# Performance work log

Hardware: AMD Instinct MI355X
Metric: run time of the kernel (lower is better)

The kernel has to match this reference:

```python
import jax, jax.numpy as jnp
import numpy as np

N, F, E, D, H, G = 65536, 256, 16, 256, 512, 256  # nodes, feat, experts(node_num), emb_dim, hidden_dim, graphs


def setup_inputs() -> dict:
    key = jax.random.key(0)
    ks = jax.random.split(key, 11)
    scale = 0.02
    return {
        "node_fea": jax.random.normal(ks[0], (N, F), jnp.float32),
        "masks": jax.random.uniform(ks[1], (N, F), jnp.float32),
        "node_type": jax.random.randint(ks[2], (N,), 0, E),
        "g_node_id": jnp.sort(jax.random.randint(ks[3], (G,), 0, N)),
        "label": jax.random.randint(ks[4], (G,), 0, 2),
        "W_emb": jax.random.normal(ks[5], (E, F, D), jnp.float32) * scale,
        "b_emb": jax.random.normal(ks[6], (E, D), jnp.float32) * scale,
        "W_hid": jax.random.normal(ks[7], (D, H), jnp.float32) * scale,
        "b_hid": jax.random.normal(ks[8], (H,), jnp.float32) * scale,
        "W_out": jax.random.normal(ks[9], (H, 2), jnp.float32) * scale,
        "b_out": jax.random.normal(ks[10], (2,), jnp.float32) * scale,
    }


def reference(node_fea, masks, node_type, g_node_id, label,
              W_emb, b_emb, W_hid, b_hid, W_out, b_out):
    # --- node_embedding: per-node type-routed linear (grouped GEMM form) ---
    xm = node_fea * masks                                   # [N, F]
    # run every expert densely, then select each node's expert output
    all_emb = jnp.einsum('nf,efd->ned', xm, W_emb) + b_emb[None]   # [N, E, D]
    emb = jnp.take_along_axis(all_emb, node_type[:, None, None], axis=1)[:, 0, :]  # [N, D]
    # --- hidden_fc (dropout in eval mode = identity) ---
    h = emb @ W_hid + b_hid                                 # [N, H]
    # --- pick first node of each batched graph ---
    g_emb = h[g_node_id]                                    # [G, H]
    # --- output layer: Linear + Softmax ---
    probs = jax.nn.softmax(g_emb @ W_out + b_out, axis=-1)  # [G, 2]
    # --- CrossEntropyLoss(reduction='sum') applied to probs (as in source) ---
    logp = jax.nn.log_softmax(probs, axis=-1)
    loss = -jnp.sum(jnp.take_along_axis(logp, label[:, None], axis=1))
    return probs, loss
```

## Files before the change

### kernel.cpp

```cpp
#include <hip/hip_runtime.h>
#include <math.h>

#define FF 256
#define EE 16
#define DD 256
#define HH 512
#define GG 256

__global__ __launch_bounds__(256) void fused_graph_kernel(
    const float* __restrict__ node_fea,
    const float* __restrict__ masks,
    const int*   __restrict__ node_type,
    const int*   __restrict__ g_node_id,
    const int*   __restrict__ label,
    const float* __restrict__ W_emb,
    const float* __restrict__ b_emb,
    const float* __restrict__ W_hid,
    const float* __restrict__ b_hid,
    const float* __restrict__ W_out,
    const float* __restrict__ b_out,
    float* __restrict__ probs_out,
    float* __restrict__ loss_ws)
{
    __shared__ float xm[FF];
    __shared__ float emb[DD];
    __shared__ float red0[4];
    __shared__ float red1[4];

    const int g = blockIdx.x;
    const int t = threadIdx.x;
    const int n = g_node_id[g];
    const int e = node_type[n];

    {
        size_t base = (size_t)n * FF + t;
        xm[t] = node_fea[base] * masks[base];
    }
    __syncthreads();

    {
        const float* __restrict__ W = W_emb + (size_t)e * FF * DD + t;
        float acc = b_emb[e * DD + t];
        #pragma unroll 8
        for (int f = 0; f < FF; ++f) {
            acc = fmaf(xm[f], W[(size_t)f * DD], acc);
        }
        emb[t] = acc;
    }
    __syncthreads();

    float z0p, z1p;
    {
        const float* __restrict__ Wh0 = W_hid + t;
        const float* __restrict__ Wh1 = W_hid + t + 256;
        float h0 = b_hid[t];
        float h1 = b_hid[t + 256];
        #pragma unroll 8
        for (int d = 0; d < DD; ++d) {
            float ed = emb[d];
            h0 = fmaf(ed, Wh0[(size_t)d * HH], h0);
            h1 = fmaf(ed, Wh1[(size_t)d * HH], h1);
        }
        z0p = h0 * W_out[2 * t + 0] + h1 * W_out[2 * (t + 256) + 0];
        z1p = h0 * W_out[2 * t + 1] + h1 * W_out[2 * (t + 256) + 1];
    }

    for (int off = 32; off > 0; off >>= 1) {
        z0p += __shfl_down(z0p, off, 64);
        z1p += __shfl_down(z1p, off, 64);
    }
    if ((t & 63) == 0) { red0[t >> 6] = z0p; red1[t >> 6] = z1p; }
    __syncthreads();

    if (t == 0) {
        float z0 = b_out[0] + red0[0] + red0[1] + red0[2] + red0[3];
        float z1 = b_out[1] + red1[0] + red1[1] + red1[2] + red1[3];
        float m  = fmaxf(z0, z1);
        float e0 = expf(z0 - m), e1 = expf(z1 - m);
        float inv = 1.0f / (e0 + e1);
        float p0 = e0 * inv, p1 = e1 * inv;
        probs_out[2 * g + 0] = p0;
        probs_out[2 * g + 1] = p1;
        float mp  = fmaxf(p0, p1);
        float lse = mp + logf(expf(p0 - mp) + expf(p1 - mp));
        float pl  = (label[g] == 0) ? p0 : p1;
        loss_ws[g] = lse - pl;
    }
}

__global__ __launch_bounds__(256) void loss_reduce_kernel(
    const float* __restrict__ loss_ws, float* __restrict__ out)
{
    __shared__ float red[4];
    int t = threadIdx.x;
    float v = loss_ws[t];
    for (int off = 32; off > 0; off >>= 1) v += __shfl_down(v, off, 64);
    if ((t & 63) == 0) red[t >> 6] = v;
    __syncthreads();
    if (t == 0) out[0] = red[0] + red[1] + red[2] + red[3];
}

extern "C" void kernel_launch(void* const* d_in, const int* in_sizes, int n_in,
                              void* d_out, int out_size, void* d_ws, size_t ws_size,
                              hipStream_t stream) {
    const float* node_fea  = (const float*)d_in[0];
    const float* masks     = (const float*)d_in[1];
    const int*   node_type = (const int*)  d_in[2];
    const int*   g_node_id = (const int*)  d_in[3];
    const int*   label     = (const int*)  d_in[4];
    const float* W_emb     = (const float*)d_in[5];
    const float* b_emb     = (const float*)d_in[6];
    const float* W_hid     = (const float*)d_in[7];
    const float* b_hid     = (const float*)d_in[8];
    const float* W_out     = (const float*)d_in[9];
    const float* b_out     = (const float*)d_in[10];

    float* out = (float*)d_out;
    float* ws  = (float*)d_ws;

    fused_graph_kernel<<<GG, 256, 0, stream>>>(
        node_fea, masks, node_type, g_node_id, label,
        W_emb, b_emb, W_hid, b_hid, W_out, b_out,
        out, ws);

    loss_reduce_kernel<<<1, 256, 0, stream>>>(ws, out + GG * 2);
}
```

Measured before the change: 161.8 us.

## Split GEMV reduction across waves with float4 vector loads

Both per-graph matrix-vector products are restructured so each of the four wavefronts handles a quarter of the reduction dimension. Each lane now computes four adjacent outputs with float4 global loads. The embedding stage writes partial sums to shared memory, which are then combined with the bias. The hidden stage keeps partial hidden vectors per wave, which is valid because the W_out projection is linear and the existing cross-wave reduction sums them. This cuts the serial dependency chain length and the number of load instructions, in exchange for extra shared memory and one extra barrier.

After: 151.8 us. 6.2% less time.

```diff
diff --git a/kernel.cpp b/kernel.cpp
--- a/kernel.cpp
+++ b/kernel.cpp
@@ -22,13 +22,17 @@
     float* __restrict__ probs_out,
     float* __restrict__ loss_ws)
 {
-    __shared__ float xm[FF];
-    __shared__ float emb[DD];
+    __shared__ __align__(16) float xm[FF];
+    __shared__ __align__(16) float part[4][DD];
+    __shared__ __align__(16) float emb[DD];
     __shared__ float red0[4];
     __shared__ float red1[4];
 
     const int g = blockIdx.x;
     const int t = threadIdx.x;
+    const int w = t >> 6;
+    const int l = t & 63;
+    const int c = l << 2;
     const int n = g_node_id[g];
     const int e = node_type[n];
 
@@ -39,37 +43,66 @@
     __syncthreads();
 
     {
-        const float* __restrict__ W = W_emb + (size_t)e * FF * DD + t;
-        float acc = b_emb[e * DD + t];
+        const float* __restrict__ Wb = W_emb + (size_t)e * FF * DD;
+        float4 acc = {0.f, 0.f, 0.f, 0.f};
         #pragma unroll 8
-        for (int f = 0; f < FF; ++f) {
-            acc = fmaf(xm[f], W[(size_t)f * DD], acc);
+        for (int i = 0; i < 64; ++i) {
+            const int f = (w << 6) + i;
+            const float s = xm[f];
+            const float4 wv = *(const float4*)(Wb + (size_t)f * DD + c);
+            acc.x = fmaf(s, wv.x, acc.x);
+            acc.y = fmaf(s, wv.y, acc.y);
+            acc.z = fmaf(s, wv.z, acc.z);
+            acc.w = fmaf(s, wv.w, acc.w);
         }
-        emb[t] = acc;
+        *(float4*)&part[w][c] = acc;
     }
+    __syncthreads();
+
+    emb[t] = part[0][t] + part[1][t] + part[2][t] + part[3][t]
+           + b_emb[e * DD + t];
     __syncthreads();
 
     float z0p, z1p;
     {
-        const float* __restrict__ Wh0 = W_hid + t;
-        const float* __restrict__ Wh1 = W_hid + t + 256;
-        float h0 = b_hid[t];
-        float h1 = b_hid[t + 256];
+        float4 ha, hb;
+        if (w == 0) {
+            ha = *(const float4*)(b_hid + c);
+            hb = *(const float4*)(b_hid + 256 + c);
+        } else {
+            ha = (float4){0.f, 0.f, 0.f, 0.f};
+            hb = (float4){0.f, 0.f, 0.f, 0.f};
+        }
         #pragma unroll 8
-        for (int d = 0; d < DD; ++d) {
-            float ed = emb[d];
-            h0 = fmaf(ed, Wh0[(size_t)d * HH], h0);
-            h1 = fmaf(ed, Wh1[(size_t)d * HH], h1);
+        for (int i = 0; i < 64; ++i) {
+            const int d = (w << 6) + i;
+            const float s = emb[d];
+            const float4 wa = *(const float4*)(W_hid + (size_t)d * HH + c);
+            const float4 wb = *(const float4*)(W_hid + (size_t)d * HH + c + 256);
+            ha.x = fmaf(s, wa.x, ha.x);
+            ha.y = fmaf(s, wa.y, ha.y);
+            ha.z = fmaf(s, wa.z, ha.z);
+            ha.w = fmaf(s, wa.w, ha.w);
+            hb.x = fmaf(s, wb.x, hb.x);
+            hb.y = fmaf(s, wb.y, hb.y);
+            hb.z = fmaf(s, wb.z, hb.z);
+            hb.w = fmaf(s, wb.w, hb.w);
         }
-        z0p = h0 * W_out[2 * t + 0] + h1 * W_out[2 * (t + 256) + 0];
-        z1p = h0 * W_out[2 * t + 1] + h1 * W_out[2 * (t + 256) + 1];
+        const float4 o0a = *(const float4*)(W_out + 2 * c);
+        const float4 o0b = *(const float4*)(W_out + 2 * c + 4);
+        const float4 o1a = *(const float4*)(W_out + 2 * (c + 256));
+        const float4 o1b = *(const float4*)(W_out + 2 * (c + 256) + 4);
+        z0p = ha.x * o0a.x + ha.y * o0a.z + ha.z * o0b.x + ha.w * o0b.z
+            + hb.x * o1a.x + hb.y * o1a.z + hb.z * o1b.x + hb.w * o1b.z;
+        z1p = ha.x * o0a.y + ha.y * o0a.w + ha.z * o0b.y + ha.w * o0b.w
+            + hb.x * o1a.y + hb.y * o1a.w + hb.z * o1b.y + hb.w * o1b.w;
     }
 
     for (int off = 32; off > 0; off >>= 1) {
         z0p += __shfl_down(z0p, off, 64);
         z1p += __shfl_down(z1p, off, 64);
     }
-    if ((t & 63) == 0) { red0[t >> 6] = z0p; red1[t >> 6] = z1p; }
+    if (l == 0) { red0[w] = z0p; red1[w] = z1p; }
     __syncthreads();
 
     if (t == 0) {
```
